# Kernel optimization log

Hardware: AMD Instinct MI355X
Metric: run time of the kernel (lower is better)

Reference implementation:

```python
import jax, jax.numpy as jnp
import numpy as np

E = 8      # num_experts
K = 2      # num_experts_per_tok
D = 1024   # n_embd
H = 1024   # expert_dim (= 2*n_embd // k)
B, T = 2, 1024


def setup_inputs() -> dict:
    key = jax.random.key(0)
    ks = jax.random.split(key, 6)
    s = 0.02  # weight init scale (keeps relu^2 activations tame)
    return {
        "x": jax.random.normal(ks[0], (B, T, D), dtype=jnp.float32),
        "gate_w": jax.random.normal(ks[1], (E, D), dtype=jnp.float32) * s,
        "lb_bias": jnp.zeros((E,), dtype=jnp.float32),
        "w1": jax.random.normal(ks[2], (E, H, D), dtype=jnp.float32) * s,
        "w2": jax.random.normal(ks[3], (E, D, H), dtype=jnp.float32) * s,
        "cfc": jax.random.normal(ks[4], (H, D), dtype=jnp.float32) * s,
        "cproj": jax.random.normal(ks[5], (D, H), dtype=jnp.float32) * s,
    }


def reference(x, gate_w, lb_bias, w1, w2, cfc, cproj):
    Bx, Tx, Dx = x.shape
    # --- Router: top-k over (logits + load-balance bias), sigmoid gating ---
    logits = jnp.einsum('btd,ed->bte', x, gate_w)               # (B,T,E)
    _, idx = jax.lax.top_k(logits + lb_bias, K)                  # (B,T,K)
    sel_logits = jnp.take_along_axis(logits, idx, axis=-1)       # (B,T,K)
    w = jax.nn.sigmoid(sel_logits)
    w = w / (jnp.sum(w, axis=-1, keepdims=True) + 1e-6)          # (B,T,K)

    # --- Dispatch/combine (dense-equivalent of the per-expert gather loop) ---
    xf = x.reshape(-1, Dx)                                       # (N,D)
    idxf = idx.reshape(-1, K)                                    # (N,K)
    wf = w.reshape(-1, K)                                        # (N,K)
    onehot = jax.nn.one_hot(idxf, E, dtype=wf.dtype)             # (N,K,E)
    we = jnp.einsum('nke,nk->ne', onehot, wf)                    # combined per-expert weight (N,E)

    hidden = jnp.square(jax.nn.relu(jnp.einsum('nd,ehd->neh', xf, w1)))  # (N,E,H)
    expert_out = jnp.einsum('neh,edh->ned', hidden, w2)                  # (N,E,D)
    moe_out = jnp.einsum('ned,ne->nd', expert_out, we).reshape(Bx, Tx, Dx)

    # --- Shared expert (always active): relu(x W1^T)^2 W2^T ---
    sh = jnp.square(jax.nn.relu(jnp.einsum('btd,hd->bth', x, cfc)))
    shared = jnp.einsum('bth,dh->btd', sh, cproj)
    return moe_out + shared
```

## Files before the change

### kernel.cpp

```cpp
#include <hip/hip_runtime.h>
#include <stdint.h>

#define D_DIM 1024
#define H_DIM 1024
#define NE 8
#define NTOK 2048
#define SB 5120
#define TOTAL_ROWS 7168
#define GEMM_BLKS 448
#define CONV2_BLKS 4608
#define M8 (8 * 1024 * 1024)

typedef __bf16 bf16;
typedef bf16 bf16x8 __attribute__((ext_vector_type(8)));
typedef float f32x4 __attribute__((ext_vector_type(4)));

#define GL16(SRC, DST)                                               \
  __builtin_amdgcn_global_load_lds(                                  \
      (const __attribute__((address_space(1))) void*)(SRC),          \
      (__attribute__((address_space(3))) void*)(DST), 16, 0, 0)

#define WS_NTILES     0
#define WS_TILE_E     64
#define WS_TILE_BASE  576
#define WS_EIDX       2048
#define WS_WTOK       18432
#define WS_TOK        34816
#define WS_SLOT       63488
#define WS_XG         131072
#define WS_HID        16777216
#define WS_W1B        33554432
#define WS_W2B        50331648
#define WS_CFCB       67108864
#define WS_CPROJB     69206016

__global__ __launch_bounds__(256) void convrouter(
    const float* __restrict__ x, const float* __restrict__ gw,
    const float* __restrict__ lb, int* __restrict__ eidx,
    float* __restrict__ wtok, bf16* __restrict__ xg,
    const float* __restrict__ w1, const float* __restrict__ cfc,
    bf16* __restrict__ w1b, bf16* __restrict__ cfcb) {
  const int bx = blockIdx.x;
  if (bx >= 512) {
    int i = ((bx - 512) * 256 + threadIdx.x) * 8;
    const float* s;
    bf16* d;
    if (i < M8) { s = w1 + i;        d = w1b + i; }
    else        { s = cfc + (i - M8); d = cfcb + (i - M8); }
    float4 a = *(const float4*)(s);
    float4 b = *(const float4*)(s + 4);
    union { uint4 v; bf16 h[8]; } t;
    t.h[0] = (bf16)a.x; t.h[1] = (bf16)a.y; t.h[2] = (bf16)a.z; t.h[3] = (bf16)a.w;
    t.h[4] = (bf16)b.x; t.h[5] = (bf16)b.y; t.h[6] = (bf16)b.z; t.h[7] = (bf16)b.w;
    *(uint4*)(d) = t.v;
    return;
  }
  const int wave = threadIdx.x >> 6;
  const int lane = threadIdx.x & 63;
  const int n = bx * 4 + wave;

  const float4* xr = (const float4*)(x + (size_t)n * D_DIM);
  float4 xv[4];
#pragma unroll
  for (int q = 0; q < 4; q++) xv[q] = xr[q * 64 + lane];

  float acc[NE];
#pragma unroll
  for (int e = 0; e < NE; e++) acc[e] = 0.f;
#pragma unroll
  for (int e = 0; e < NE; e++) {
    const float4* gr = (const float4*)(gw + e * D_DIM);
#pragma unroll
    for (int q = 0; q < 4; q++) {
      float4 g = gr[q * 64 + lane];
      acc[e] += xv[q].x * g.x + xv[q].y * g.y + xv[q].z * g.z + xv[q].w * g.w;
    }
  }

  bf16* dst = xg + (size_t)n * D_DIM;
#pragma unroll
  for (int q = 0; q < 4; q++) {
    union { ushort4 u; bf16 h[4]; } t;
    t.h[0] = (bf16)xv[q].x; t.h[1] = (bf16)xv[q].y;
    t.h[2] = (bf16)xv[q].z; t.h[3] = (bf16)xv[q].w;
    *(ushort4*)(dst + (q * 64 + lane) * 4) = t.u;
  }

#pragma unroll
  for (int e = 0; e < NE; e++)
#pragma unroll
    for (int off = 32; off > 0; off >>= 1) acc[e] += __shfl_xor(acc[e], off, 64);

  if (lane == 0) {
    float b[NE];
#pragma unroll
    for (int e = 0; e < NE; e++) b[e] = acc[e] + lb[e];
    int i0 = 0; float v0 = b[0];
#pragma unroll
    for (int e = 1; e < NE; e++) if (b[e] > v0) { v0 = b[e]; i0 = e; }
    int i1 = -1; float v1 = -3.4e38f;
#pragma unroll
    for (int e = 0; e < NE; e++) if (e != i0 && b[e] > v1) { v1 = b[e]; i1 = e; }
    float s0 = 1.f / (1.f + expf(-acc[i0]));
    float s1 = 1.f / (1.f + expf(-acc[i1]));
    float s = s0 + s1 + 1e-6f;
    eidx[n * 2] = i0;     wtok[n * 2] = s0 / s;
    eidx[n * 2 + 1] = i1; wtok[n * 2 + 1] = s1 / s;
  }
}

__global__ __launch_bounds__(256) void assign_kernel(
    const int* __restrict__ eidx, int* __restrict__ tE, int* __restrict__ tB,
    int* __restrict__ ntiles, int* __restrict__ tok,
    int* __restrict__ slotIdx) {
  __shared__ int segCnt[64][NE];
  __shared__ int segBase[64][NE];
  const int tid = threadIdx.x;
  const int wave = tid >> 6, lane = tid & 63;
  const unsigned long long below = (lane == 0) ? 0ull : ((~0ull) >> (64 - lane));

  int e16[16], pr16[16];
#pragma unroll
  for (int t = 0; t < 16; t++) {
    const int r = t * 256 + tid;
    const int seg = t * 4 + wave;
    const int e = eidx[r];
    int prior = 0;
#pragma unroll
    for (int ee = 0; ee < NE; ee++) {
      unsigned long long m = __ballot(e == ee);
      if (e == ee) prior = __popcll(m & below);
      if (lane == ee) segCnt[seg][ee] = __popcll(m);
    }
    e16[t] = e; pr16[t] = prior;
  }

  for (int s = tid; s < TOTAL_ROWS; s += 256) {
    tok[s] = (s < SB) ? 0 : (s - SB);
  }
  __syncthreads();

  if (wave == 0) {
    int v[NE], inc[NE];
#pragma unroll
    for (int e = 0; e < NE; e++) { v[e] = segCnt[lane][e]; inc[e] = v[e]; }
#pragma unroll
    for (int off = 1; off < 64; off <<= 1) {
#pragma unroll
      for (int e = 0; e < NE; e++) {
        int u = __shfl_up(inc[e], off);
        if (lane >= off) inc[e] += u;
      }
    }
    int tot[NE];
#pragma unroll
    for (int e = 0; e < NE; e++) tot[e] = __shfl(inc[e], 63);
    int offsL[NE]; int b = 0;
#pragma unroll
    for (int e = 0; e < NE; e++) { offsL[e] = b; b += ((tot[e] + 127) >> 7) << 7; }
#pragma unroll
    for (int e = 0; e < NE; e++) segBase[lane][e] = offsL[e] + (inc[e] - v[e]);
    if (lane == 0) {
      int nt = 0;
      for (int e = 0; e < NE; e++) {
        int t128 = (tot[e] + 127) >> 7;
        for (int t = 0; t < t128; t++) { tE[nt] = e; tB[nt] = offsL[e] + t * 128; nt++; }
      }
      for (int t = 0; t < 16; t++) { tE[nt] = NE; tB[nt] = SB + t * 128; nt++; }
      ntiles[0] = nt;
      ntiles[1] = nt;
    }
  }
  __syncthreads();

#pragma unroll
  for (int t = 0; t < 16; t++) {
    const int r = t * 256 + tid;
    const int seg = t * 4 + wave;
    const int slot = segBase[seg][e16[t]] + pr16[t];
    tok[slot] = r >> 1;
    slotIdx[r] = slot;
  }
}

template <int MODE>
__global__ __launch_bounds__(256) void moe_gemm(
    const bf16* __restrict__ Ab, const bf16* __restrict__ We,
    const bf16* __restrict__ Ws, const int* __restrict__ tE,
    const int* __restrict__ tB, const int* __restrict__ ntp,
    bf16* __restrict__ Cout, const int* __restrict__ tok,
    const float* __restrict__ cvs1, const float* __restrict__ cvs2,
    bf16* __restrict__ cvd1, bf16* __restrict__ cvd2) {
  if (MODE == 0 && blockIdx.x >= GEMM_BLKS) {
    int i = ((blockIdx.x - GEMM_BLKS) * 256 + threadIdx.x) * 8;
    const float* s;
    bf16* d;
    if (i < M8) { s = cvs1 + i;        d = cvd1 + i; }
    else        { s = cvs2 + (i - M8); d = cvd2 + (i - M8); }
    float4 a = *(const float4*)(s);
    float4 b = *(const float4*)(s + 4);
    union { uint4 v; bf16 h[8]; } t;
    t.h[0] = (bf16)a.x; t.h[1] = (bf16)a.y; t.h[2] = (bf16)a.z; t.h[3] = (bf16)a.w;
    t.h[4] = (bf16)b.x; t.h[5] = (bf16)b.y; t.h[6] = (bf16)b.z; t.h[7] = (bf16)b.w;
    *(uint4*)(d) = t.v;
    return;
  }

  const int per = ntp[1];
  const int g = blockIdx.x & 7, idx = blockIdx.x >> 3;
  if (idx >= per) return;
  const int p = g * per + idx;
  const int mslot = p >> 3;
  const int n0 = (p & 7) * 128;
  const int e = tE[mslot];
  const int base = tB[mslot];
  const bf16* Bp = (e < NE) ? (We + (size_t)e * (H_DIM * D_DIM)) : Ws;

  __shared__ bf16 As[3 * 4096];
  __shared__ bf16 Bs[3 * 4096];

  const int tid = threadIdx.x;
  const int wave = tid >> 6, lane = tid & 63;

  const int rS = tid >> 2, sS = tid & 3;
  const int cS = sS ^ ((rS >> 1) & 3);
  size_t rowA1, rowA2;
  if (MODE == 0) { rowA1 = tok[base + rS]; rowA2 = tok[base + 64 + rS]; }
  else           { rowA1 = base + rS;      rowA2 = base + 64 + rS; }
  const bf16* gA1 = Ab + rowA1 * 1024 + cS * 8;
  const bf16* gA2 = Ab + rowA2 * 1024 + cS * 8;
  const bf16* gB1 = Bp + (size_t)(n0 + rS) * 1024 + cS * 8;
  const bf16* gB2 = Bp + (size_t)(n0 + 64 + rS) * 1024 + cS * 8;
  bf16* laBase = As + tid * 8;
  bf16* lbBase = Bs + tid * 8;

  const int wm = (wave >> 1) * 64, wn = (wave & 1) * 64;
  const int fr = lane & 15, chk = lane >> 4;
  int aOff[4], bOff[4];
#pragma unroll
  for (int i = 0; i < 4; i++) {
    const int r = wm + i * 16 + fr;
    aOff[i] = r * 32 + ((chk ^ ((r >> 1) & 3)) * 8);
  }
#pragma unroll
  for (int j = 0; j < 4; j++) {
    const int r = wn + j * 16 + fr;
    bOff[j] = r * 32 + ((chk ^ ((r >> 1) & 3)) * 8);
  }

  const f32x4 zero = {0.f, 0.f, 0.f, 0.f};
  f32x4 acc[4][4];
#pragma unroll
  for (int i = 0; i < 4; i++)
#pragma unroll
    for (int j = 0; j < 4; j++) acc[i][j] = zero;

#pragma unroll
  for (int t = 0; t < 3; ++t) {
    const int ko = t * 32;
    const int bo = t * 4096;
    GL16(gA1 + ko, laBase + bo);
    GL16(gA2 + ko, laBase + bo + 2048);
    GL16(gB1 + ko, lbBase + bo);
    GL16(gB2 + ko, lbBase + bo + 2048);
  }

  int cur = 0;
#define GEMM_ITER(KT, VMSTR, ISSUE)                                           \
  {                                                                           \
    asm volatile("s_waitcnt vmcnt(" VMSTR ")" ::: "memory");                  \
    __builtin_amdgcn_s_barrier();              \
    __builtin_amdgcn_sched_barrier(0);                                        \
    bf16x8 af[4], bv[4];                                                      \
    _Pragma("unroll") for (int i = 0; i < 4; i++)                             \
        af[i] = *(const bf16x8*)&As[cur * 4096 + aOff[i]];                    \
    _Pragma("unroll") for (int j = 0; j < 4; j++)                             \
        bv[j] = *(const bf16x8*)&Bs[cur * 4096 + bOff[j]];                    \
    asm volatile("s_waitcnt lgkmcnt(0)" ::: "memory");                        \
    __builtin_amdgcn_s_barrier();             \
    __builtin_amdgcn_sched_barrier(0);                                        \
    if (ISSUE) {                                                              \
      const int ko = ((KT) + 3) * 32;                                         \
      const int bo = cur * 4096;                                              \
      GL16(gA1 + ko, laBase + bo);                                            \
      GL16(gA2 + ko, laBase + bo + 2048);                                     \
      GL16(gB1 + ko, lbBase + bo);                                            \
      GL16(gB2 + ko, lbBase + bo + 2048);                                     \
    }                                                                         \
    __builtin_amdgcn_s_setprio(1);                                            \
    _Pragma("unroll") for (int i = 0; i < 4; i++)                             \
      _Pragma("unroll") for (int j = 0; j < 4; j++)                           \
          acc[i][j] = __builtin_amdgcn_mfma_f32_16x16x32_bf16(                \
              af[i], bv[j], acc[i][j], 0, 0, 0);                              \
    __builtin_amdgcn_s_setprio(0);                                            \
    cur = (cur == 2) ? 0 : cur + 1;                                           \
  }

  for (int kt = 0; kt < 30; ++kt) GEMM_ITER(kt, "8", (kt < 29));
  GEMM_ITER(30, "4", false);
  GEMM_ITER(31, "0", false);
#undef GEMM_ITER

  const int rbase = (lane >> 4) * 4;
#pragma unroll
  for (int i = 0; i < 4; i++) {
#pragma unroll
    for (int j = 0; j < 4; j++) {
      const int col = n0 + wn + j * 16 + fr;
#pragma unroll
      for (int r = 0; r < 4; r++) {
        const int orow = wm + i * 16 + rbase + r;
        float v = acc[i][j][r];
        if (MODE == 0) v = v > 0.f ? v * v : 0.f;
        Cout[(size_t)(base + orow) * 1024 + col] = (bf16)v;
      }
    }
  }
}

__global__ __launch_bounds__(256) void combine_kernel(
    const bf16* __restrict__ eo, const int* __restrict__ slotIdx,
    const float* __restrict__ wtok, float* __restrict__ out) {
  const int t = blockIdx.x;
  const int c = threadIdx.x * 4;
  const int s0 = slotIdx[t * 2], s1 = slotIdx[t * 2 + 1];
  const float w0 = wtok[t * 2], w1 = wtok[t * 2 + 1];
  union U { uint2 v; bf16 h[4]; };
  U a, b, sh;
  a.v  = *(const uint2*)(eo + (size_t)s0 * 1024 + c);
  b.v  = *(const uint2*)(eo + (size_t)s1 * 1024 + c);
  sh.v = *(const uint2*)(eo + (size_t)(SB + t) * 1024 + c);
  float4 o;
  o.x = w0 * (float)a.h[0] + w1 * (float)b.h[0] + (float)sh.h[0];
  o.y = w0 * (float)a.h[1] + w1 * (float)b.h[1] + (float)sh.h[1];
  o.z = w0 * (float)a.h[2] + w1 * (float)b.h[2] + (float)sh.h[2];
  o.w = w0 * (float)a.h[3] + w1 * (float)b.h[3] + (float)sh.h[3];
  *(float4*)(out + (size_t)t * 1024 + c) = o;
}

extern "C" void kernel_launch(void* const* d_in, const int* in_sizes, int n_in,
                              void* d_out, int out_size, void* d_ws,
                              size_t ws_size, hipStream_t stream) {
  const float* x     = (const float*)d_in[0];
  const float* gw    = (const float*)d_in[1];
  const float* lb    = (const float*)d_in[2];
  const float* w1    = (const float*)d_in[3];
  const float* w2    = (const float*)d_in[4];
  const float* cfc   = (const float*)d_in[5];
  const float* cproj = (const float*)d_in[6];
  float* out = (float*)d_out;
  char* ws = (char*)d_ws;

  int*   ntl   = (int*)(ws + WS_NTILES);
  int*   tE    = (int*)(ws + WS_TILE_E);
  int*   tB    = (int*)(ws + WS_TILE_BASE);
  int*   eidx  = (int*)(ws + WS_EIDX);
  float* wtok  = (float*)(ws + WS_WTOK);
  int*   tok   = (int*)(ws + WS_TOK);
  int*   slotI = (int*)(ws + WS_SLOT);
  bf16*  xg    = (bf16*)(ws + WS_XG);
  bf16*  hid   = (bf16*)(ws + WS_HID);
  bf16*  w1b   = (bf16*)(ws + WS_W1B);
  bf16*  w2b   = (bf16*)(ws + WS_W2B);
  bf16*  cfcb  = (bf16*)(ws + WS_CFCB);
  bf16*  cprojb= (bf16*)(ws + WS_CPROJB);

  convrouter<<<5120, 256, 0, stream>>>(x, gw, lb, eidx, wtok, xg,
                                       w1, cfc, w1b, cfcb);
  assign_kernel<<<1, 256, 0, stream>>>(eidx, tE, tB, ntl, tok, slotI);

  moe_gemm<0><<<GEMM_BLKS + CONV2_BLKS, 256, 0, stream>>>(
      xg, w1b, cfcb, tE, tB, ntl, hid, tok, w2, cproj, w2b, cprojb);
  moe_gemm<1><<<GEMM_BLKS, 256, 0, stream>>>(
      hid, w2b, cprojb, tE, tB, ntl, xg, tok, nullptr, nullptr, nullptr, nullptr);
  combine_kernel<<<NTOK, 256, 0, stream>>>(xg, slotI, wtok, out);
}
```

Baseline: 82.93 us.

## Deepen LDS ring to four stages and double-buffer register fragments

Moves the GEMM main loop from a 3-stage to a 4-stage LDS ring. It also preloads the next k-tile's A/B fragments into a second register set while the MFMAs for the current tile run, which removes one barrier per iteration. The goal is to overlap LDS reads with matrix math and hide more global-load latency. In exchange, LDS use rises to 64KB per block and register pressure roughly doubles for the fragments, which may lower occupancy.

```diff
diff --git a/kernel.cpp b/kernel.cpp
--- a/kernel.cpp
+++ b/kernel.cpp
@@ -216,8 +216,8 @@
   const int base = tB[mslot];
   const bf16* Bp = (e < NE) ? (We + (size_t)e * (H_DIM * D_DIM)) : Ws;
 
-  __shared__ bf16 As[3 * 4096];
-  __shared__ bf16 Bs[3 * 4096];
+  __shared__ bf16 As[4 * 4096];
+  __shared__ bf16 Bs[4 * 4096];
 
   const int tid = threadIdx.x;
   const int wave = tid >> 6, lane = tid & 63;
@@ -256,7 +256,7 @@
     for (int j = 0; j < 4; j++) acc[i][j] = zero;
 
 #pragma unroll
-  for (int t = 0; t < 3; ++t) {
+  for (int t = 0; t < 4; ++t) {
     const int ko = t * 32;
     const int bo = t * 4096;
     GL16(gA1 + ko, laBase + bo);
@@ -265,41 +265,64 @@
     GL16(gB2 + ko, lbBase + bo + 2048);
   }
 
-  int cur = 0;
-#define GEMM_ITER(KT, VMSTR, ISSUE)                                           \
+  bf16x8 afA[4], bvA[4], afB[4], bvB[4];
+
+  asm volatile("s_waitcnt vmcnt(12)" ::: "memory");
+  __builtin_amdgcn_s_barrier();
+  __builtin_amdgcn_sched_barrier(0);
+#pragma unroll
+  for (int i = 0; i < 4; i++) afA[i] = *(const bf16x8*)&As[aOff[i]];
+#pragma unroll
+  for (int j = 0; j < 4; j++) bvA[j] = *(const bf16x8*)&Bs[bOff[j]];
+  asm volatile("s_waitcnt lgkmcnt(0)" ::: "memory");
+  __builtin_amdgcn_sched_barrier(0);
+
+#define GEMM_ITER(KT, VMS, ISSUE, AFC, BVC, AFN, BVN)                         \
   {                                                                           \
-    asm volatile("s_waitcnt vmcnt(" VMSTR ")" ::: "memory");                  \
-    __builtin_amdgcn_s_barrier();              \
-    __builtin_amdgcn_sched_barrier(0);                                        \
-    bf16x8 af[4], bv[4];                                                      \
-    _Pragma("unroll") for (int i = 0; i < 4; i++)                             \
-        af[i] = *(const bf16x8*)&As[cur * 4096 + aOff[i]];                    \
-    _Pragma("unroll") for (int j = 0; j < 4; j++)                             \
-        bv[j] = *(const bf16x8*)&Bs[cur * 4096 + bOff[j]];                    \
-    asm volatile("s_waitcnt lgkmcnt(0)" ::: "memory");                        \
-    __builtin_amdgcn_s_barrier();             \
+    asm volatile("s_waitcnt vmcnt(" VMS ")" ::: "memory");                    \
+    __builtin_amdgcn_s_barrier();                                             \
     __builtin_amdgcn_sched_barrier(0);                                        \
     if (ISSUE) {                                                              \
-      const int ko = ((KT) + 3) * 32;                                         \
-      const int bo = cur * 4096;                                              \
+      const int ko = ((KT) + 4) * 32;                                         \
+      const int bo = ((KT) & 3) * 4096;                                       \
       GL16(gA1 + ko, laBase + bo);                                            \
       GL16(gA2 + ko, laBase + bo + 2048);                                     \
       GL16(gB1 + ko, lbBase + bo);                                            \
       GL16(gB2 + ko, lbBase + bo + 2048);                                     \
     }                                                                         \
+    {                                                                         \
+      const int br = (((KT) + 1) & 3) * 4096;                                 \
+      _Pragma("unroll") for (int i = 0; i < 4; i++)                           \
+          AFN[i] = *(const bf16x8*)&As[br + aOff[i]];                         \
+      _Pragma("unroll") for (int j = 0; j < 4; j++)                           \
+          BVN[j] = *(const bf16x8*)&Bs[br + bOff[j]];                         \
+    }                                                                         \
     __builtin_amdgcn_s_setprio(1);                                            \
     _Pragma("unroll") for (int i = 0; i < 4; i++)                             \
       _Pragma("unroll") for (int j = 0; j < 4; j++)                           \
           acc[i][j] = __builtin_amdgcn_mfma_f32_16x16x32_bf16(                \
-              af[i], bv[j], acc[i][j], 0, 0, 0);                              \
+              AFC[i], BVC[j], acc[i][j], 0, 0, 0);                            \
     __builtin_amdgcn_s_setprio(0);                                            \
-    cur = (cur == 2) ? 0 : cur + 1;                                           \
-  }
-
-  for (int kt = 0; kt < 30; ++kt) GEMM_ITER(kt, "8", (kt < 29));
-  GEMM_ITER(30, "4", false);
-  GEMM_ITER(31, "0", false);
+    asm volatile("s_waitcnt lgkmcnt(0)" ::: "memory");                        \
+    __builtin_amdgcn_sched_barrier(0);                                        \
+  }
+
+  for (int kt = 0; kt < 28; kt += 2) {
+    GEMM_ITER(kt,     "8", true, afA, bvA, afB, bvB);
+    GEMM_ITER(kt + 1, "8", true, afB, bvB, afA, bvA);
+  }
+  GEMM_ITER(28, "8", false, afA, bvA, afB, bvB);
+  GEMM_ITER(29, "4", false, afB, bvB, afA, bvA);
+  GEMM_ITER(30, "0", false, afA, bvA, afB, bvB);
 #undef GEMM_ITER
+  __builtin_amdgcn_s_setprio(1);
+#pragma unroll
+  for (int i = 0; i < 4; i++)
+#pragma unroll
+    for (int j = 0; j < 4; j++)
+      acc[i][j] = __builtin_amdgcn_mfma_f32_16x16x32_bf16(afB[i], bvB[j],
+                                                          acc[i][j], 0, 0, 0);
+  __builtin_amdgcn_s_setprio(0);
 
   const int rbase = (lane >> 4) * 4;
 #pragma unroll
```

Measured after the change: 89.51 us. 1.08x slower.

## Stream fp32 W1/cfc directly into first GEMM with in-register bf16 conversion

Applied to the files above, without the earlier changes.

The first expert GEMM now reads fp32 W1 and shared-expert weights straight from global memory into registers and converts them to bf16 before each MFMA. This removes the separate fp32-to-bf16 conversion pass over W1 and cfc in the router kernel, along with its write and re-read of a bf16 copy. The GEMM drops the LDS triple-buffered global_load_lds pipeline for direct per-lane register double-buffering, and the second GEMM is split into its own non-templated kernel. In exchange, each block reads twice as many weight bytes, there is no LDS reuse across waves, and the kernel adds per-lane gathers and conversion ALU work.

```diff
diff --git a/kernel.cpp b/kernel.cpp
--- a/kernel.cpp
+++ b/kernel.cpp
@@ -37,24 +37,8 @@
 __global__ __launch_bounds__(256) void convrouter(
     const float* __restrict__ x, const float* __restrict__ gw,
     const float* __restrict__ lb, int* __restrict__ eidx,
-    float* __restrict__ wtok, bf16* __restrict__ xg,
-    const float* __restrict__ w1, const float* __restrict__ cfc,
-    bf16* __restrict__ w1b, bf16* __restrict__ cfcb) {
+    float* __restrict__ wtok, bf16* __restrict__ xg) {
   const int bx = blockIdx.x;
-  if (bx >= 512) {
-    int i = ((bx - 512) * 256 + threadIdx.x) * 8;
-    const float* s;
-    bf16* d;
-    if (i < M8) { s = w1 + i;        d = w1b + i; }
-    else        { s = cfc + (i - M8); d = cfcb + (i - M8); }
-    float4 a = *(const float4*)(s);
-    float4 b = *(const float4*)(s + 4);
-    union { uint4 v; bf16 h[8]; } t;
-    t.h[0] = (bf16)a.x; t.h[1] = (bf16)a.y; t.h[2] = (bf16)a.z; t.h[3] = (bf16)a.w;
-    t.h[4] = (bf16)b.x; t.h[5] = (bf16)b.y; t.h[6] = (bf16)b.z; t.h[7] = (bf16)b.w;
-    *(uint4*)(d) = t.v;
-    return;
-  }
   const int wave = threadIdx.x >> 6;
   const int lane = threadIdx.x & 63;
   const int n = bx * 4 + wave;
@@ -183,15 +167,14 @@
   }
 }
 
-template <int MODE>
-__global__ __launch_bounds__(256) void moe_gemm(
-    const bf16* __restrict__ Ab, const bf16* __restrict__ We,
-    const bf16* __restrict__ Ws, const int* __restrict__ tE,
+__global__ __launch_bounds__(256, 2) void moe_gemm_stream(
+    const bf16* __restrict__ Ab, const float* __restrict__ W1,
+    const float* __restrict__ Cfc, const int* __restrict__ tE,
     const int* __restrict__ tB, const int* __restrict__ ntp,
     bf16* __restrict__ Cout, const int* __restrict__ tok,
     const float* __restrict__ cvs1, const float* __restrict__ cvs2,
     bf16* __restrict__ cvd1, bf16* __restrict__ cvd2) {
-  if (MODE == 0 && blockIdx.x >= GEMM_BLKS) {
+  if (blockIdx.x >= GEMM_BLKS) {
     int i = ((blockIdx.x - GEMM_BLKS) * 256 + threadIdx.x) * 8;
     const float* s;
     bf16* d;
@@ -214,6 +197,100 @@
   const int n0 = (p & 7) * 128;
   const int e = tE[mslot];
   const int base = tB[mslot];
+  const float* Bp = (e < NE) ? (W1 + (size_t)e * (H_DIM * D_DIM)) : Cfc;
+
+  const int tid = threadIdx.x;
+  const int wave = tid >> 6, lane = tid & 63;
+  const int wm = (wave >> 1) * 64, wn = (wave & 1) * 64;
+  const int fr = lane & 15, chk = lane >> 4;
+
+  const bf16* pa[4];
+#pragma unroll
+  for (int i = 0; i < 4; i++) {
+    const int slot = base + wm + i * 16 + fr;
+    pa[i] = Ab + (size_t)tok[slot] * 1024 + chk * 8;
+  }
+  const float* pb[4];
+#pragma unroll
+  for (int j = 0; j < 4; j++)
+    pb[j] = Bp + (size_t)(n0 + wn + j * 16 + fr) * 1024 + chk * 8;
+
+  const f32x4 zero = {0.f, 0.f, 0.f, 0.f};
+  f32x4 acc[4][4];
+#pragma unroll
+  for (int i = 0; i < 4; i++)
+#pragma unroll
+    for (int j = 0; j < 4; j++) acc[i][j] = zero;
+
+  bf16x8 aA[4], aB[4];
+  float4 lA[4], hA[4], lB[4], hB[4];
+
+#define LOADSET(AS, BLO, BHI, KT)                                             \
+  {                                                                           \
+    _Pragma("unroll") for (int i = 0; i < 4; i++)                             \
+        AS[i] = *(const bf16x8*)(pa[i] + (KT) * 32);                          \
+    _Pragma("unroll") for (int j = 0; j < 4; j++) {                           \
+      BLO[j] = *(const float4*)(pb[j] + (KT) * 32);                           \
+      BHI[j] = *(const float4*)(pb[j] + (KT) * 32 + 4);                       \
+    }                                                                         \
+  }
+#define CVTMFMA(AS, BLO, BHI)                                                 \
+  {                                                                           \
+    bf16x8 bv[4];                                                             \
+    _Pragma("unroll") for (int j = 0; j < 4; j++) {                           \
+      union { bf16x8 v; bf16 h[8]; } c;                                       \
+      c.h[0] = (bf16)BLO[j].x; c.h[1] = (bf16)BLO[j].y;                       \
+      c.h[2] = (bf16)BLO[j].z; c.h[3] = (bf16)BLO[j].w;                       \
+      c.h[4] = (bf16)BHI[j].x; c.h[5] = (bf16)BHI[j].y;                       \
+      c.h[6] = (bf16)BHI[j].z; c.h[7] = (bf16)BHI[j].w;                       \
+      bv[j] = c.v;                                                            \
+    }                                                                         \
+    _Pragma("unroll") for (int i = 0; i < 4; i++)                             \
+      _Pragma("unroll") for (int j = 0; j < 4; j++)                           \
+          acc[i][j] = __builtin_amdgcn_mfma_f32_16x16x32_bf16(                \
+              AS[i], bv[j], acc[i][j], 0, 0, 0);                              \
+  }
+
+  LOADSET(aA, lA, hA, 0);
+  for (int kt = 0; kt < 32; kt += 2) {
+    if (kt + 1 < 32) LOADSET(aB, lB, hB, kt + 1);
+    CVTMFMA(aA, lA, hA);
+    if (kt + 2 < 32) LOADSET(aA, lA, hA, kt + 2);
+    CVTMFMA(aB, lB, hB);
+  }
+#undef LOADSET
+#undef CVTMFMA
+
+  const int rbase = (lane >> 4) * 4;
+#pragma unroll
+  for (int i = 0; i < 4; i++) {
+#pragma unroll
+    for (int j = 0; j < 4; j++) {
+      const int col = n0 + wn + j * 16 + fr;
+#pragma unroll
+      for (int r = 0; r < 4; r++) {
+        const int orow = wm + i * 16 + rbase + r;
+        float v = acc[i][j][r];
+        v = v > 0.f ? v * v : 0.f;
+        Cout[(size_t)(base + orow) * 1024 + col] = (bf16)v;
+      }
+    }
+  }
+}
+
+__global__ __launch_bounds__(256) void moe_gemm2(
+    const bf16* __restrict__ Ab, const bf16* __restrict__ We,
+    const bf16* __restrict__ Ws, const int* __restrict__ tE,
+    const int* __restrict__ tB, const int* __restrict__ ntp,
+    bf16* __restrict__ Cout) {
+  const int per = ntp[1];
+  const int g = blockIdx.x & 7, idx = blockIdx.x >> 3;
+  if (idx >= per) return;
+  const int p = g * per + idx;
+  const int mslot = p >> 3;
+  const int n0 = (p & 7) * 128;
+  const int e = tE[mslot];
+  const int base = tB[mslot];
   const bf16* Bp = (e < NE) ? (We + (size_t)e * (H_DIM * D_DIM)) : Ws;
 
   __shared__ bf16 As[3 * 4096];
@@ -224,11 +301,8 @@
 
   const int rS = tid >> 2, sS = tid & 3;
   const int cS = sS ^ ((rS >> 1) & 3);
-  size_t rowA1, rowA2;
-  if (MODE == 0) { rowA1 = tok[base + rS]; rowA2 = tok[base + 64 + rS]; }
-  else           { rowA1 = base + rS;      rowA2 = base + 64 + rS; }
-  const bf16* gA1 = Ab + rowA1 * 1024 + cS * 8;
-  const bf16* gA2 = Ab + rowA2 * 1024 + cS * 8;
+  const bf16* gA1 = Ab + (size_t)(base + rS) * 1024 + cS * 8;
+  const bf16* gA2 = Ab + (size_t)(base + 64 + rS) * 1024 + cS * 8;
   const bf16* gB1 = Bp + (size_t)(n0 + rS) * 1024 + cS * 8;
   const bf16* gB2 = Bp + (size_t)(n0 + 64 + rS) * 1024 + cS * 8;
   bf16* laBase = As + tid * 8;
@@ -265,11 +339,11 @@
     GL16(gB2 + ko, lbBase + bo + 2048);
   }
 
-  int cur = 0;
 #define GEMM_ITER(KT, VMSTR, ISSUE)                                           \
   {                                                                           \
+    const int cur = (KT) % 3;                                                 \
     asm volatile("s_waitcnt vmcnt(" VMSTR ")" ::: "memory");                  \
-    __builtin_amdgcn_s_barrier();              \
+    __builtin_amdgcn_s_barrier();                                             \
     __builtin_amdgcn_sched_barrier(0);                                        \
     bf16x8 af[4], bv[4];                                                      \
     _Pragma("unroll") for (int i = 0; i < 4; i++)                             \
@@ -277,7 +351,7 @@
     _Pragma("unroll") for (int j = 0; j < 4; j++)                             \
         bv[j] = *(const bf16x8*)&Bs[cur * 4096 + bOff[j]];                    \
     asm volatile("s_waitcnt lgkmcnt(0)" ::: "memory");                        \
-    __builtin_amdgcn_s_barrier();             \
+    __builtin_amdgcn_s_barrier();                                             \
     __builtin_amdgcn_sched_barrier(0);                                        \
     if (ISSUE) {                                                              \
       const int ko = ((KT) + 3) * 32;                                         \
@@ -293,7 +367,6 @@
           acc[i][j] = __builtin_amdgcn_mfma_f32_16x16x32_bf16(                \
               af[i], bv[j], acc[i][j], 0, 0, 0);                              \
     __builtin_amdgcn_s_setprio(0);                                            \
-    cur = (cur == 2) ? 0 : cur + 1;                                           \
   }
 
   for (int kt = 0; kt < 30; ++kt) GEMM_ITER(kt, "8", (kt < 29));
@@ -310,9 +383,7 @@
 #pragma unroll
       for (int r = 0; r < 4; r++) {
         const int orow = wm + i * 16 + rbase + r;
-        float v = acc[i][j][r];
-        if (MODE == 0) v = v > 0.f ? v * v : 0.f;
-        Cout[(size_t)(base + orow) * 1024 + col] = (bf16)v;
+        Cout[(size_t)(base + orow) * 1024 + col] = (bf16)acc[i][j][r];
       }
     }
   }
@@ -360,18 +431,15 @@
   int*   slotI = (int*)(ws + WS_SLOT);
   bf16*  xg    = (bf16*)(ws + WS_XG);
   bf16*  hid   = (bf16*)(ws + WS_HID);
-  bf16*  w1b   = (bf16*)(ws + WS_W1B);
   bf16*  w2b   = (bf16*)(ws + WS_W2B);
-  bf16*  cfcb  = (bf16*)(ws + WS_CFCB);
   bf16*  cprojb= (bf16*)(ws + WS_CPROJB);
 
-  convrouter<<<5120, 256, 0, stream>>>(x, gw, lb, eidx, wtok, xg,
-                                       w1, cfc, w1b, cfcb);
+  convrouter<<<512, 256, 0, stream>>>(x, gw, lb, eidx, wtok, xg);
   assign_kernel<<<1, 256, 0, stream>>>(eidx, tE, tB, ntl, tok, slotI);
 
-  moe_gemm<0><<<GEMM_BLKS + CONV2_BLKS, 256, 0, stream>>>(
-      xg, w1b, cfcb, tE, tB, ntl, hid, tok, w2, cproj, w2b, cprojb);
-  moe_gemm<1><<<GEMM_BLKS, 256, 0, stream>>>(
-      hid, w2b, cprojb, tE, tB, ntl, xg, tok, nullptr, nullptr, nullptr, nullptr);
+  moe_gemm_stream<<<GEMM_BLKS + CONV2_BLKS, 256, 0, stream>>>(
+      xg, w1, cfc, tE, tB, ntl, hid, tok, w2, cproj, w2b, cprojb);
+  moe_gemm2<<<GEMM_BLKS, 256, 0, stream>>>(
+      hid, w2b, cprojb, tE, tB, ntl, xg);
   combine_kernel<<<NTOK, 256, 0, stream>>>(xg, slotI, wtok, out);
 }
```

New measurement: 143.2 us. 1.73x slower.
